# Optimization experiments

Hardware: AMD Instinct MI355X
Metric: run time of the kernel (lower is better)

The kernel has to match this reference:

```python
import jax, jax.numpy as jnp
import numpy as np

N, E, D, H, C = 100000, 1600000, 64, 8, 10
NEG_SLOPE = 0.2


def setup_inputs() -> dict:
    key = jax.random.key(0)
    ks = jax.random.split(key, 20)
    rn = lambda k, sh: jax.random.normal(k, sh, jnp.float32) * 0.1
    return dict(
        x=jax.random.normal(ks[0], (N, D), jnp.float32),
        edge_index=jax.random.randint(ks[1], (2, E), 0, N),
        gcnK_W=rn(ks[2], (D, D)), gcnK_b=rn(ks[3], (D,)),
        gcnV_W=rn(ks[4], (D, D)), gcnV_b=rn(ks[5], (D,)),
        super_Q=rn(ks[6], (C, D)),
        mha_in_w=rn(ks[7], (3 * D, D)), mha_in_b=rn(ks[8], (3 * D,)),
        mha_out_w=rn(ks[9], (D, D)), mha_out_b=rn(ks[10], (D,)),
        gat_W=rn(ks[11], (D, D)), gat_Wc=rn(ks[12], (D, D)),
        gat_a_src=rn(ks[13], (D,)), gat_a_dst=rn(ks[14], (D,)),
        gat_b=rn(ks[15], (D,)),
        t1_W=rn(ks[16], (D, 2 * D)), t1_b=rn(ks[17], (2 * D,)),
        t2_W=rn(ks[18], (2 * D, D)), t2_b=rn(ks[19], (D,)),
    )


def _gcn(x, W, b, src, dst, norm_e):
    # PyG GCNConv: symmetric-normalized aggregation over (A + I)
    h = x @ W  # [N, D]
    agg = jax.ops.segment_sum(h[src] * norm_e[:, None], dst, num_segments=N)
    return agg + b


def _mha(q, k, v, in_w, in_b, out_w, out_b):
    # torch.nn.MultiheadAttention (unbatched), eval mode (dropout off)
    L, n, hd = q.shape[0], k.shape[0], D // H
    Wq, Wk, Wv = jnp.split(in_w, 3, axis=0)
    bq, bk, bv = jnp.split(in_b, 3)
    scale = 1.0 / float(np.sqrt(hd))
    qh = ((q @ Wq.T + bq) * scale).reshape(L, H, hd).transpose(1, 0, 2)  # [H,L,hd]
    kh = (k @ Wk.T + bk).reshape(n, H, hd).transpose(1, 0, 2)            # [H,n,hd]
    vh = (v @ Wv.T + bv).reshape(n, H, hd).transpose(1, 0, 2)
    attn = jax.nn.softmax(jnp.einsum('hld,hnd->hln', qh, kh), axis=-1)
    o = jnp.einsum('hln,hnd->hld', attn, vh).transpose(1, 0, 2).reshape(L, D)
    return o @ out_w.T + out_b


def _context_gat(x, src, dst, context, W, Wc, a_src, a_dst, b):
    # context-conditioned GAT: per-edge logits use node terms + global context gate
    h = x @ W
    c = context @ Wc  # [D]
    s_src = h @ (a_src + c)  # context modulates source attention vector
    s_dst = h @ a_dst
    logits = jax.nn.leaky_relu(s_src[src] + s_dst[dst], NEG_SLOPE)  # [E]
    m = jax.ops.segment_max(logits, dst, num_segments=N)
    ex = jnp.exp(logits - m[dst])
    denom = jax.ops.segment_sum(ex, dst, num_segments=N)
    alpha = ex / (denom[dst] + 1e-16)
    out = jax.ops.segment_sum(alpha[:, None] * h[src], dst, num_segments=N)
    return out + b


def reference(x, edge_index, gcnK_W, gcnK_b, gcnV_W, gcnV_b, super_Q,
              mha_in_w, mha_in_b, mha_out_w, mha_out_b,
              gat_W, gat_Wc, gat_a_src, gat_a_dst, gat_b,
              t1_W, t1_b, t2_W, t2_b):
    src, dst = edge_index[0], edge_index[1]
    loop = jnp.arange(N)
    srcl = jnp.concatenate([src, loop])
    dstl = jnp.concatenate([dst, loop])
    deg = jax.ops.segment_sum(jnp.ones_like(srcl, jnp.float32), dstl, num_segments=N)
    dinv = jnp.where(deg > 0, 1.0 / jnp.sqrt(deg), 0.0)
    norm_e = dinv[srcl] * dinv[dstl]
    x_K = _gcn(x, gcnK_W, gcnK_b, srcl, dstl, norm_e)
    x_V = _gcn(x, gcnV_W, gcnV_b, srcl, dstl, norm_e)
    cluster = _mha(super_Q, x_K, x_V, mha_in_w, mha_in_b, mha_out_w, mha_out_b)  # [C, D]
    context = jnp.mean(cluster, axis=0)  # [D]
    g = _context_gat(x_V, src, dst, context, gat_W, gat_Wc, gat_a_src, gat_a_dst, gat_b)
    h1 = jax.nn.relu(g @ t1_W + t1_b)
    return jax.nn.relu(h1 @ t2_W + t2_b)
```

## Files before the change

### kernel.cpp

```cpp
#include <hip/hip_runtime.h>
#include <hip/hip_bf16.h>
#include <stdint.h>

#define NN 100000
#define EE 1600000
#define NBK 391
#define CHUNK 4096
#define NCB 98
#define NPROJ 1563
#define NS 32

#define FMA4(xi, vv, a, base)                      \
  a[(base)+0] = fmaf((xi), (vv).x, a[(base)+0]);   \
  a[(base)+1] = fmaf((xi), (vv).y, a[(base)+1]);   \
  a[(base)+2] = fmaf((xi), (vv).z, a[(base)+2]);   \
  a[(base)+3] = fmaf((xi), (vv).w, a[(base)+3]);

typedef __attribute__((ext_vector_type(8))) short bf16x8;
typedef __attribute__((ext_vector_type(4))) float f32x4;
typedef __attribute__((ext_vector_type(2))) float f32x2;
union FragU { uint4 u; bf16x8 h; };

__device__ inline unsigned pack_bf2(float a, float b) {
  __hip_bfloat162 t;
  t.x = __float2bfloat16(a);
  t.y = __float2bfloat16(b);
  return *reinterpret_cast<unsigned*>(&t);
}

__device__ inline f32x2 unpk2(unsigned u) {
  f32x2 r;
  r.x = __uint_as_float(u << 16);
  r.y = __uint_as_float(u & 0xffff0000u);
  return r;
}

__launch_bounds__(256)
__global__ void k_hist(const int* __restrict__ ei, int* __restrict__ histmat) {
  __shared__ int hist[NCB];
  int t = threadIdx.x;
  if (t < NCB) hist[t] = 0;
  __syncthreads();
  int base = blockIdx.x * CHUNK;
  int nb = EE - base; if (nb > CHUNK) nb = CHUNK;
  for (int k = t; k < nb; k += 256)
    atomicAdd(&hist[ei[EE + base + k] >> 10], 1);
  __syncthreads();
  if (t < NCB) histmat[blockIdx.x * NCB + t] = hist[t];
}

__launch_bounds__(256)
__global__ void k_sumcb(const int* __restrict__ histmat, int* __restrict__ cbsum) {
  __shared__ int red[4];
  int cb = blockIdx.x, t = threadIdx.x;
  int s = 0;
  for (int blk = t; blk < NBK; blk += 256) s += histmat[blk * NCB + cb];
#pragma unroll
  for (int off = 32; off > 0; off >>= 1) s += __shfl_down(s, off);
  if ((t & 63) == 0) red[t >> 6] = s;
  __syncthreads();
  if (t == 0) cbsum[cb] = red[0] + red[1] + red[2] + red[3];
}

__launch_bounds__(512)
__global__ void k_ppos(const int* __restrict__ histmat, const int* __restrict__ cbsum,
                       int* __restrict__ bstart, int* __restrict__ offsets,
                       int* __restrict__ ppos) {
  __shared__ int sm[512];
  __shared__ int sb[128];
  int cb = blockIdx.x, t = threadIdx.x;
  if (t < 128) sb[t] = (t < NCB) ? cbsum[t] : 0;
  __syncthreads();
  for (int off = 1; off < 128; off <<= 1) {
    int x = (t < 128 && t >= off) ? sb[t - off] : 0;
    __syncthreads();
    if (t < 128) sb[t] += x;
    __syncthreads();
  }
  int bs = (cb == 0) ? 0 : sb[cb - 1];
  if (t == 0) bstart[cb] = bs;
  if (cb == 0 && t == 0) { bstart[NCB] = EE; offsets[NN] = EE; }
  int v = (t < NBK) ? histmat[t * NCB + cb] : 0;
  sm[t] = v;
  __syncthreads();
  for (int off = 1; off < 512; off <<= 1) {
    int x = (t >= off) ? sm[t - off] : 0;
    __syncthreads();
    sm[t] += x;
    __syncthreads();
  }
  if (t < NBK) ppos[cb * NBK + t] = bs + sm[t] - v;
}

__launch_bounds__(256)
__global__ void k_fill_b(const int* __restrict__ ei, const int* __restrict__ ppos,
                         unsigned* __restrict__ brec) {
  __shared__ int hist[NCB], binstart[NCB], bincur[NCB], pbase[NCB];
  __shared__ unsigned lbuf[CHUNK];
  __shared__ unsigned char cbArr[CHUNK];
  int t = threadIdx.x;
  int base = blockIdx.x * CHUNK;
  int nb = EE - base; if (nb > CHUNK) nb = CHUNK;
  if (t < NCB) { hist[t] = 0; pbase[t] = ppos[t * NBK + blockIdx.x]; }
  __syncthreads();
  unsigned rec[16]; int rcb[16]; int cnt = 0;
  for (int k = t; k < nb; k += 256) {
    int s = ei[base + k], d = ei[EE + base + k];
    rec[cnt] = (unsigned)s | ((unsigned)(d & 1023) << 17);
    rcb[cnt] = d >> 10;
    atomicAdd(&hist[rcb[cnt]], 1);
    cnt++;
  }
  __syncthreads();
  if (t < NCB) binstart[t] = hist[t];
  __syncthreads();
  for (int off = 1; off < NCB; off <<= 1) {
    int v = (t < NCB && t >= off) ? binstart[t - off] : 0;
    __syncthreads();
    if (t < NCB) binstart[t] += v;
    __syncthreads();
  }
  if (t < NCB) { binstart[t] -= hist[t]; bincur[t] = 0; }
  __syncthreads();
  for (int i = 0; i < cnt; i++) {
    int c = rcb[i];
    int pos = atomicAdd(&bincur[c], 1);
    int p = binstart[c] + pos;
    lbuf[p] = rec[i];
    cbArr[p] = (unsigned char)c;
  }
  __syncthreads();
  for (int i = t; i < nb; i += 256) {
    int c = cbArr[i];
    brec[pbase[c] + (i - binstart[c])] = lbuf[i];
  }
}

__launch_bounds__(1024)
__global__ void k_fill_c(const unsigned* __restrict__ brec, const int* __restrict__ bstart,
                         int* __restrict__ csr, int* __restrict__ offsets,
                         float* __restrict__ dinv) {
  __shared__ int cnt[1024], sm[1024];
  int cbk = blockIdx.x, t = threadIdx.x;
  int nb0 = cbk << 10;
  int nn = NN - nb0; if (nn > 1024) nn = 1024;
  cnt[t] = 0;
  __syncthreads();
  int e0 = bstart[cbk], e1 = bstart[cbk + 1];
  for (int j = e0 + t; j < e1; j += 1024)
    atomicAdd(&cnt[brec[j] >> 17], 1);
  __syncthreads();
  int cv = cnt[t];
  sm[t] = cv;
  __syncthreads();
  for (int off = 1; off < 1024; off <<= 1) {
    int v = (t >= off) ? sm[t - off] : 0;
    __syncthreads();
    sm[t] += v;
    __syncthreads();
  }
  sm[t] -= cv;
  if (t < nn) {
    offsets[nb0 + t] = e0 + sm[t];
    dinv[nb0 + t] = rsqrtf((float)(cv + 1));
  }
  cnt[t] = 0;
  __syncthreads();
  for (int j = e0 + t; j < e1; j += 1024) {
    unsigned r = brec[j];
    int dl = r >> 17;
    int p = atomicAdd(&cnt[dl], 1);
    csr[e0 + sm[dl] + p] = r & 0x1FFFF;
  }
}

__global__ void k_prep(const float* __restrict__ x, const float* __restrict__ dinv,
                       unsigned* __restrict__ xbf2) {
  int i = blockIdx.x * 256 + threadIdx.x;
  if (i >= NN * 32) return;
  float dv = dinv[i >> 5];
  float2 v = ((const float2*)x)[i];
  xbf2[i] = pack_bf2(v.x * dv, v.y * dv);
}

__launch_bounds__(256)
__global__ void k_agg_x(const unsigned* __restrict__ xbf2, const int* __restrict__ offsets,
                        const int* __restrict__ csr, const float* __restrict__ dinv,
                        unsigned* __restrict__ axb) {
  int gid = blockIdx.x * 256 + threadIdx.x;
  int n = gid >> 6;
  if (n >= NN) return;
  int lane = gid & 63, q = lane & 7, grp = lane >> 3;
  int e0 = offsets[n], e1 = offsets[n + 1];
  float dv = dinv[n];
  f32x2 a2[4];
#pragma unroll
  for (int i = 0; i < 4; i++) a2[i] = (f32x2){0.f, 0.f};
  if (grp == 0) {
    uint4 u = ((const uint4*)(xbf2 + (size_t)n * 32))[q];
    unsigned uu[4] = {u.x, u.y, u.z, u.w};
#pragma unroll
    for (int p = 0; p < 4; p++) a2[p] += unpk2(uu[p]);
  }
  int b2 = e0;
  for (; b2 + 8 < e1; b2 += 16) {
    int j0 = b2 + grp, j1 = j0 + 8;
    int s0 = csr[j0];
    bool ok1 = j1 < e1;
    int s1 = ok1 ? csr[j1] : s0;
    uint4 u0 = ((const uint4*)(xbf2 + (size_t)s0 * 32))[q];
    uint4 u1 = ((const uint4*)(xbf2 + (size_t)s1 * 32))[q];
    unsigned w0[4] = {u0.x, u0.y, u0.z, u0.w};
    unsigned w1[4] = {u1.x, u1.y, u1.z, u1.w};
#pragma unroll
    for (int p = 0; p < 4; p++) a2[p] += unpk2(w0[p]);
    if (ok1) {
#pragma unroll
      for (int p = 0; p < 4; p++) a2[p] += unpk2(w1[p]);
    }
  }
  for (; b2 < e1; b2 += 8) {
    int j = b2 + grp;
    if (j < e1) {
      int s = csr[j];
      uint4 u = ((const uint4*)(xbf2 + (size_t)s * 32))[q];
      unsigned uu[4] = {u.x, u.y, u.z, u.w};
#pragma unroll
      for (int p = 0; p < 4; p++) a2[p] += unpk2(uu[p]);
    }
  }
#pragma unroll
  for (int i = 0; i < 4; i++) {
    a2[i].x += __shfl_xor(a2[i].x, 8);
    a2[i].x += __shfl_xor(a2[i].x, 16);
    a2[i].x += __shfl_xor(a2[i].x, 32);
    a2[i].y += __shfl_xor(a2[i].y, 8);
    a2[i].y += __shfl_xor(a2[i].y, 16);
    a2[i].y += __shfl_xor(a2[i].y, 32);
  }
  if (lane < 8) {
    uint4 u;
    u.x = pack_bf2(a2[0].x * dv, a2[0].y * dv);
    u.y = pack_bf2(a2[1].x * dv, a2[1].y * dv);
    u.z = pack_bf2(a2[2].x * dv, a2[2].y * dv);
    u.w = pack_bf2(a2[3].x * dv, a2[3].y * dv);
    ((uint4*)(axb + (size_t)n * 32))[q] = u;
  }
}

__launch_bounds__(256)
__global__ void k_fusew(const float* __restrict__ gcnK_W, const float* __restrict__ gcnK_b,
                        const float* __restrict__ gcnV_W, const float* __restrict__ gcnV_b,
                        const float* __restrict__ mha_in_w, const float* __restrict__ mha_in_b,
                        const float* __restrict__ gat_W, const float* __restrict__ sQ,
                        unsigned* __restrict__ Wt, float* __restrict__ bb) {
  __shared__ float sW1[64 * 65];
  __shared__ float sW2[64 * 65];
  __shared__ float sW3[64 * 65];
  __shared__ float sqq[640], qhs[640], Ms[5120], kb[64];
  int blk = blockIdx.x, t = threadIdx.x;
  const float scale = 0.35355339059327373f;
  if (blk < 16) {
    for (int i = t; i < 4096; i += 256) sW1[(i >> 6) * 65 + (i & 63)] = gcnV_W[i];
    if (blk < 8) {
      for (int i = t; i < 512; i += 256) sW2[i] = mha_in_w[(128 + blk * 8) * 64 + i];
    } else {
      for (int i = t; i < 4096; i += 256) sW2[(i >> 6) * 65 + (i & 63)] = gat_W[i];
    }
    __syncthreads();
    int idx = blk * 256 + t;
    int d = idx >> 5, kp = idx & 31;
    float v2[2];
#pragma unroll
    for (int u2 = 0; u2 < 2; u2++) {
      int k = kp * 2 + u2;
      float s = 0.f;
      if (d < 64) {
        int r = d & 7;
        for (int j = 0; j < 64; j++) s = fmaf(sW1[k * 65 + j], sW2[r * 64 + j], s);
      } else {
        int c = d - 64;
        for (int j = 0; j < 64; j++) s = fmaf(sW1[k * 65 + j], sW2[j * 65 + c], s);
      }
      v2[u2] = s;
    }
    Wt[idx] = pack_bf2(v2[0], v2[1]);
    if (t < 8) {
      if (blk < 8) {
        int d0 = blk * 8 + t;
        float s = mha_in_b[128 + d0];
        for (int j = 0; j < 64; j++) s = fmaf(gcnV_b[j], sW2[t * 64 + j], s);
        bb[d0] = s;
      } else {
        int c = (blk - 8) * 8 + t;
        float s = 0.f;
        for (int j = 0; j < 64; j++) s = fmaf(gcnV_b[j], sW2[j * 65 + c], s);
        bb[64 + c] = s;
      }
    }
  } else {
    for (int i = t; i < 4096; i += 256) {
      int r = i >> 6, c = i & 63;
      sW1[r * 65 + c] = gcnK_W[i];
      sW2[r * 65 + c] = mha_in_w[64 * 64 + i];
      sW3[r * 65 + c] = mha_in_w[i];
    }
    for (int i = t; i < 640; i += 256) sqq[i] = sQ[i];
    __syncthreads();
    for (int e = t; e < 640; e += 256) {
      int lv = e >> 6, c = e & 63;
      float acc = mha_in_b[c];
      for (int i = 0; i < 64; i++) acc = fmaf(sqq[lv * 64 + i], sW3[c * 65 + i], acc);
      qhs[e] = acc * scale;
    }
    if (t < 64) {
      float s = mha_in_b[64 + t];
      for (int j = 0; j < 64; j++) s = fmaf(gcnK_b[j], sW2[t * 65 + j], s);
      kb[t] = s;
    }
    __syncthreads();
    for (int e = t; e < 5120; e += 256) {
      int j = e / 80, hl = e % 80;
      int h = hl / 10, lv = hl % 10;
      float s = 0.f;
#pragma unroll
      for (int c = 0; c < 8; c++) {
        int cp = h * 8 + c;
        s = fmaf(sW2[cp * 65 + j], qhs[lv * 64 + cp], s);
      }
      Ms[j * 80 + hl] = s;
    }
    if (t < 80) {
      int h = t / 10, lv = t % 10;
      float s = 0.f;
#pragma unroll
      for (int c = 0; c < 8; c++) {
        int cp = h * 8 + c;
        s = fmaf(kb[cp], qhs[lv * 64 + cp], s);
      }
      bb[128 + t] = s;
    }
    __syncthreads();
    for (int e = t; e < 2560; e += 256) {
      int hl = e >> 5, kp = e & 31;
      float v2[2];
#pragma unroll
      for (int u2 = 0; u2 < 2; u2++) {
        int k = kp * 2 + u2;
        float s = 0.f;
        for (int j = 0; j < 64; j++) s = fmaf(sW1[k * 65 + j], Ms[j * 80 + hl], s);
        v2[u2] = s;
      }
      Wt[(128 + hl) * 32 + kp] = pack_bf2(v2[0], v2[1]);
    }
  }
}

__launch_bounds__(256)
__global__ void k_proj(const unsigned* __restrict__ axb, const unsigned* __restrict__ Wt,
                       const float* __restrict__ bb, const float* __restrict__ a_dst,
                       unsigned* __restrict__ hGb, float* __restrict__ s_dstv,
                       float* __restrict__ part) {
  __shared__ float red[4][720];
  int t = threadIdx.x;
  int wid = t >> 6, l = t & 63;
  int l15 = l & 15, lg = l >> 4;
  int base = blockIdx.x * 64;
  int rowbase = base + wid * 16;

  FragU a0, a1;
  {
    int r = rowbase + l15;
    if (r < NN) {
      const uint4* p = (const uint4*)(axb + (size_t)r * 32);
      a0.u = p[lg];
      a1.u = p[4 + lg];
    } else {
      a0.u = make_uint4(0u, 0u, 0u, 0u);
      a1.u = a0.u;
    }
  }
  f32x4 acc[13];
#pragma unroll
  for (int ct = 0; ct < 13; ct++) acc[ct] = (f32x4){0.f, 0.f, 0.f, 0.f};
#pragma unroll
  for (int ct = 0; ct < 13; ct++) {
    const uint4* wp = (const uint4*)(Wt + (size_t)(ct * 16 + l15) * 32);
    FragU b0, b1;
    b0.u = wp[lg];
    b1.u = wp[4 + lg];
    acc[ct] = __builtin_amdgcn_mfma_f32_16x16x32_bf16(a0.h, b0.h, acc[ct], 0, 0, 0);
    acc[ct] = __builtin_amdgcn_mfma_f32_16x16x32_bf16(a1.h, b1.h, acc[ct], 0, 0, 0);
  }

  float sdp[4] = {0.f, 0.f, 0.f, 0.f};
  __hip_bfloat16* hgp = (__hip_bfloat16*)hGb;
#pragma unroll
  for (int gt = 0; gt < 4; gt++) {
    int col = gt * 16 + l15;
    float bias = bb[64 + col];
    float ad = a_dst[col];
#pragma unroll
    for (int r = 0; r < 4; r++) {
      float hg = acc[4 + gt][r] + bias;
      sdp[r] = fmaf(hg, ad, sdp[r]);
      int row = rowbase + lg * 4 + r;
      if (row < NN) hgp[(size_t)row * 64 + col] = __float2bfloat16(hg);
    }
  }
#pragma unroll
  for (int r = 0; r < 4; r++) {
    float v = sdp[r];
    v += __shfl_xor(v, 1); v += __shfl_xor(v, 2);
    v += __shfl_xor(v, 4); v += __shfl_xor(v, 8);
    int row = rowbase + lg * 4 + r;
    if (l15 == 0 && row < NN) s_dstv[row] = v;
  }

  float wz[5][4];
#pragma unroll
  for (int zt = 0; zt < 5; zt++) {
    int zcol = zt * 16 + l15;
    float bias = bb[128 + zcol];
    float sp = 0.f;
#pragma unroll
    for (int r = 0; r < 4; r++) {
      int row = rowbase + lg * 4 + r;
      float z = acc[8 + zt][r] + bias;
      float w = (row < NN) ? __expf(z) : 0.f;
      wz[zt][r] = w;
      sp += w;
    }
    sp += __shfl_xor(sp, 16);
    sp += __shfl_xor(sp, 32);
    if (l < 16) {
      int h = zcol / 10, lv = zcol % 10;
      red[wid][h * 90 + lv] = sp;
    }
  }

  int sA = (l15 + 32 * lg) & 63;
  int sB2 = (sA + 16) & 63;
  bool loK = (lg < 2);
  FragU af[5];
#pragma unroll
  for (int zt = 0; zt < 5; zt++) {
    unsigned wlo = pack_bf2(wz[zt][0], wz[zt][1]);
    unsigned whi = pack_bf2(wz[zt][2], wz[zt][3]);
    unsigned f0 = __shfl(wlo, sA), f1 = __shfl(whi, sA);
    unsigned f2 = __shfl(wlo, sB2), f3 = __shfl(whi, sB2);
    af[zt].u.x = loK ? f0 : 0u;
    af[zt].u.y = loK ? f1 : 0u;
    af[zt].u.z = loK ? f2 : 0u;
    af[zt].u.w = loK ? f3 : 0u;
  }
#pragma unroll
  for (int vt = 0; vt < 4; vt++) {
    float bias = bb[vt * 16 + l15];
    unsigned vlo = pack_bf2(acc[vt][0] + bias, acc[vt][1] + bias);
    unsigned vhi = pack_bf2(acc[vt][2] + bias, acc[vt][3] + bias);
    FragU bf;
    {
      unsigned f0 = __shfl(vlo, sA), f1 = __shfl(vhi, sA);
      unsigned f2 = __shfl(vlo, sB2), f3 = __shfl(vhi, sB2);
      bf.u.x = loK ? f0 : 0u;
      bf.u.y = loK ? f1 : 0u;
      bf.u.z = loK ? f2 : 0u;
      bf.u.w = loK ? f3 : 0u;
    }
    f32x4 oacc[5];
#pragma unroll
    for (int zt = 0; zt < 5; zt++) {
      oacc[zt] = (f32x4){0.f, 0.f, 0.f, 0.f};
      oacc[zt] = __builtin_amdgcn_mfma_f32_16x16x32_bf16(af[zt].h, bf.h, oacc[zt], 0, 0, 0);
    }
#pragma unroll
    for (int zt = 0; zt < 5; zt++) {
#pragma unroll
      for (int r = 0; r < 4; r++) {
        int hl = zt * 16 + lg * 4 + r;
        int h = hl / 10, lv = hl - h * 10;
        if (vt * 2 + (l15 >> 3) == h)
          red[wid][h * 90 + 10 + lv * 8 + (l15 & 7)] = oacc[zt][r];
      }
    }
  }

  __syncthreads();
  for (int j = t; j < 720; j += 256) {
    float v = red[0][j] + red[1][j] + red[2][j] + red[3][j];
    part[(size_t)blockIdx.x * 720 + j] = v;
  }
}

__launch_bounds__(256)
__global__ void k_mred1(const float* __restrict__ part, float* __restrict__ part2) {
  int blk = blockIdx.x, t = threadIdx.x;
  int per = (NPROJ + NS - 1) / NS;
  int b0 = blk * per, b1 = b0 + per; if (b1 > NPROJ) b1 = NPROJ;
  float v0 = 0.f, v1 = 0.f, v2 = 0.f;
  for (int b = b0; b < b1; b++) {
    const float* row = part + (size_t)b * 720;
    v0 += row[t];
    if (t + 256 < 720) v1 += row[t + 256];
    if (t + 512 < 720) v2 += row[t + 512];
  }
  part2[(size_t)blk * 720 + t] = v0;
  if (t + 256 < 720) part2[(size_t)blk * 720 + t + 256] = v1;
  if (t + 512 < 720) part2[(size_t)blk * 720 + t + 512] = v2;
}

__global__ void k_context(const float* __restrict__ part2, const float* __restrict__ out_w,
                          const float* __restrict__ out_b, const float* __restrict__ a_src,
                          const float* __restrict__ gat_Wc, float* __restrict__ aeff) {
  __shared__ float po[640], cl[640], ctx[64], ac[720];
  int t = threadIdx.x;
  for (int j = t; j < 720; j += 640) {
    float v = 0.f;
#pragma unroll
    for (int s = 0; s < NS; s++) v += part2[(size_t)s * 720 + j];
    int cg = j / 90, r = j % 90;
    ac[(r < 10) ? (cg * 10 + r) : (80 + cg * 80 + (r - 10))] = v;
  }
  __syncthreads();
  {
    int h = t / 80, r = t % 80, l = r >> 3, j = r & 7;
    po[l * 64 + h * 8 + j] = ac[80 + t] / ac[h * 10 + l];
  }
  __syncthreads();
  {
    int l = t >> 6, d = t & 63;
    float v = out_b[d];
    for (int c = 0; c < 64; c++) v = fmaf(po[l * 64 + c], out_w[d * 64 + c], v);
    cl[t] = v;
  }
  __syncthreads();
  if (t < 64) {
    float m = 0.f;
#pragma unroll
    for (int l = 0; l < 10; l++) m += cl[l * 64 + t];
    ctx[t] = m * 0.1f;
  }
  __syncthreads();
  if (t < 64) {
    float v = a_src[t];
    for (int i = 0; i < 64; i++) v = fmaf(ctx[i], gat_Wc[i * 64 + t], v);
    aeff[t] = v;
  }
}

__launch_bounds__(256)
__global__ void k_ssrc(const unsigned* __restrict__ hGb, const float* __restrict__ aeff,
                       float* __restrict__ s_src) {
  int gid = blockIdx.x * 256 + threadIdx.x;
  int n = gid >> 6, lane = gid & 63;
  if (n >= NN) return;
  const __hip_bfloat16* hp = (const __hip_bfloat16*)hGb;
  float v = __bfloat162float(hp[(size_t)n * 64 + lane]) * aeff[lane];
#pragma unroll
  for (int off = 32; off > 0; off >>= 1) v += __shfl_xor(v, off);
  if (lane == 0) s_src[n] = v;
}

__launch_bounds__(256)
__global__ void k_gat(const int* __restrict__ offsets, const int* __restrict__ csr,
                      const float* __restrict__ s_src, const float* __restrict__ s_dstv,
                      const unsigned* __restrict__ hGb, const float* __restrict__ gat_b,
                      unsigned* __restrict__ gb) {
  int gid = blockIdx.x * 256 + threadIdx.x;
  int n = gid >> 6;
  if (n >= NN) return;
  int lane = gid & 63, q = lane & 7, grp = lane >> 3;
  int e0 = offsets[n], e1 = offsets[n + 1];
  float sd = s_dstv[n];
  float den = 0.f;
  f32x2 a2[4];
#pragma unroll
  for (int i = 0; i < 4; i++) a2[i] = (f32x2){0.f, 0.f};
  int b2 = e0;
  for (; b2 + 8 < e1; b2 += 16) {
    int j0 = b2 + grp, j1 = j0 + 8;
    int s0 = csr[j0];
    bool ok1 = j1 < e1;
    int s1 = ok1 ? csr[j1] : s0;
    float z0 = s_src[s0] + sd;
    float z1 = s_src[s1] + sd;
    uint4 u0 = ((const uint4*)(hGb + (size_t)s0 * 32))[q];
    uint4 u1 = ((const uint4*)(hGb + (size_t)s1 * 32))[q];
    unsigned w0[4] = {u0.x, u0.y, u0.z, u0.w};
    unsigned w1[4] = {u1.x, u1.y, u1.z, u1.w};
    z0 = z0 > 0.f ? z0 : 0.2f * z0;
    float ex0 = __expf(z0);
    den += ex0;
    f32x2 e0v = (f32x2){ex0, ex0};
#pragma unroll
    for (int p = 0; p < 4; p++) a2[p] = e0v * unpk2(w0[p]) + a2[p];
    if (ok1) {
      z1 = z1 > 0.f ? z1 : 0.2f * z1;
      float ex1 = __expf(z1);
      den += ex1;
      f32x2 e1v = (f32x2){ex1, ex1};
#pragma unroll
      for (int p = 0; p < 4; p++) a2[p] = e1v * unpk2(w1[p]) + a2[p];
    }
  }
  for (; b2 < e1; b2 += 8) {
    int j = b2 + grp;
    if (j < e1) {
      int s = csr[j];
      float z = s_src[s] + sd;
      z = z > 0.f ? z : 0.2f * z;
      float ex = __expf(z);
      den += ex;
      uint4 u = ((const uint4*)(hGb + (size_t)s * 32))[q];
      unsigned uu[4] = {u.x, u.y, u.z, u.w};
      f32x2 ev = (f32x2){ex, ex};
#pragma unroll
      for (int p = 0; p < 4; p++) a2[p] = ev * unpk2(uu[p]) + a2[p];
    }
  }
  den += __shfl_xor(den, 8);
  den += __shfl_xor(den, 16);
  den += __shfl_xor(den, 32);
#pragma unroll
  for (int i = 0; i < 4; i++) {
    a2[i].x += __shfl_xor(a2[i].x, 8);
    a2[i].x += __shfl_xor(a2[i].x, 16);
    a2[i].x += __shfl_xor(a2[i].x, 32);
    a2[i].y += __shfl_xor(a2[i].y, 8);
    a2[i].y += __shfl_xor(a2[i].y, 16);
    a2[i].y += __shfl_xor(a2[i].y, 32);
  }
  float inv = 1.f / (den + 1e-16f);
  if (lane < 8) {
    uint4 u;
    u.x = pack_bf2(a2[0].x * inv + gat_b[q * 8 + 0], a2[0].y * inv + gat_b[q * 8 + 1]);
    u.y = pack_bf2(a2[1].x * inv + gat_b[q * 8 + 2], a2[1].y * inv + gat_b[q * 8 + 3]);
    u.z = pack_bf2(a2[2].x * inv + gat_b[q * 8 + 4], a2[2].y * inv + gat_b[q * 8 + 5]);
    u.w = pack_bf2(a2[3].x * inv + gat_b[q * 8 + 6], a2[3].y * inv + gat_b[q * 8 + 7]);
    ((uint4*)(gb + (size_t)n * 32))[q] = u;
  }
}

__launch_bounds__(256)
__global__ void k_mlp1(const unsigned* __restrict__ gb, const float* __restrict__ W1,
                       const float* __restrict__ b1, unsigned* __restrict__ h1b) {
  __shared__ float sX[32 * 65];
  __shared__ float sW[64 * 128];
  __shared__ float sb[128];
  int t = threadIdx.x;
  int base = blockIdx.x * 32;
  for (int i = t; i < 8192; i += 256) sW[i] = W1[i];
  if (t < 128) sb[t] = b1[t];
  for (int idx = t; idx < 32 * 8; idx += 256) {
    int rl = idx >> 3, c8 = idx & 7;
    int row = base + rl;
    uint4 u = (row < NN) ? ((const uint4*)(gb + (size_t)row * 32))[c8]
                         : make_uint4(0u, 0u, 0u, 0u);
    unsigned uu[4] = {u.x, u.y, u.z, u.w};
    float* dst = sX + rl * 65 + c8 * 8;
#pragma unroll
    for (int p = 0; p < 4; p++) {
      __hip_bfloat162 v = *reinterpret_cast<__hip_bfloat162*>(&uu[p]);
      dst[2 * p] = __bfloat162float(v.x);
      dst[2 * p + 1] = __bfloat162float(v.y);
    }
  }
  __syncthreads();
  int cg = t & 15, rg = t >> 4;
  int r0 = rg * 2;
  float a0[8], a1[8];
#pragma unroll
  for (int i = 0; i < 8; i++) { a0[i] = 0.f; a1[i] = 0.f; }
  const float4* W4 = (const float4*)sW;
#pragma unroll 4
  for (int i = 0; i < 64; i++) {
    float x0 = sX[r0 * 65 + i];
    float x1 = sX[(r0 + 1) * 65 + i];
    float4 w0 = W4[i * 32 + cg * 2], w1 = W4[i * 32 + cg * 2 + 1];
    FMA4(x0, w0, a0, 0); FMA4(x0, w1, a0, 4);
    FMA4(x1, w0, a1, 0); FMA4(x1, w1, a1, 4);
  }
#pragma unroll
  for (int r = 0; r < 2; r++) {
    int row = base + r0 + r;
    if (row >= NN) continue;
    float* a = r ? a1 : a0;
    float h[8];
#pragma unroll
    for (int c = 0; c < 8; c++) h[c] = fmaxf(a[c] + sb[cg * 8 + c], 0.f);
    uint4 u;
    u.x = pack_bf2(h[0], h[1]);
    u.y = pack_bf2(h[2], h[3]);
    u.z = pack_bf2(h[4], h[5]);
    u.w = pack_bf2(h[6], h[7]);
    ((uint4*)(h1b + (size_t)row * 64))[cg] = u;
  }
}

__launch_bounds__(256)
__global__ void k_mlp2(const unsigned* __restrict__ h1b, const float* __restrict__ W2,
                       const float* __restrict__ b2, float* __restrict__ out) {
  __shared__ unsigned sH[64 * 65];
  __shared__ float sW[128 * 64];
  __shared__ float sb[64];
  int t = threadIdx.x;
  int base = blockIdx.x * 64;
  for (int i = t; i < 8192; i += 256) sW[i] = W2[i];
  if (t < 64) sb[t] = b2[t];
  for (int idx = t; idx < 64 * 16; idx += 256) {
    int rl = idx >> 4, c4 = idx & 15;
    int row = base + rl;
    uint4 v = (row < NN) ? ((const uint4*)h1b)[(size_t)row * 16 + c4]
                         : make_uint4(0u, 0u, 0u, 0u);
    sH[rl * 65 + 4 * c4 + 0] = v.x;
    sH[rl * 65 + 4 * c4 + 1] = v.y;
    sH[rl * 65 + 4 * c4 + 2] = v.z;
    sH[rl * 65 + 4 * c4 + 3] = v.w;
  }
  __syncthreads();
  int cg = t & 7, rg = t >> 3;
  int r0 = rg * 2;
  float a0[8], a1[8];
#pragma unroll
  for (int i = 0; i < 8; i++) { a0[i] = 0.f; a1[i] = 0.f; }
  const float4* W4 = (const float4*)sW;
#pragma unroll 2
  for (int kp = 0; kp < 64; kp++) {
    unsigned u0 = sH[r0 * 65 + kp];
    unsigned u1 = sH[(r0 + 1) * 65 + kp];
    float x0a = __uint_as_float(u0 << 16), x0b = __uint_as_float(u0 & 0xffff0000u);
    float x1a = __uint_as_float(u1 << 16), x1b = __uint_as_float(u1 & 0xffff0000u);
    int k0 = 2 * kp, k1 = 2 * kp + 1;
    float4 wa0 = W4[k0 * 16 + cg * 2], wa1 = W4[k0 * 16 + cg * 2 + 1];
    float4 wb0 = W4[k1 * 16 + cg * 2], wb1 = W4[k1 * 16 + cg * 2 + 1];
    FMA4(x0a, wa0, a0, 0); FMA4(x0a, wa1, a0, 4);
    FMA4(x0b, wb0, a0, 0); FMA4(x0b, wb1, a0, 4);
    FMA4(x1a, wa0, a1, 0); FMA4(x1a, wa1, a1, 4);
    FMA4(x1b, wb0, a1, 0); FMA4(x1b, wb1, a1, 4);
  }
#pragma unroll
  for (int r = 0; r < 2; r++) {
    int row = base + r0 + r;
    if (row >= NN) continue;
    float* a = r ? a1 : a0;
    float4* op = (float4*)(out + (size_t)row * 64 + cg * 8);
    op[0] = make_float4(fmaxf(a[0] + sb[cg * 8 + 0], 0.f), fmaxf(a[1] + sb[cg * 8 + 1], 0.f),
                        fmaxf(a[2] + sb[cg * 8 + 2], 0.f), fmaxf(a[3] + sb[cg * 8 + 3], 0.f));
    op[1] = make_float4(fmaxf(a[4] + sb[cg * 8 + 4], 0.f), fmaxf(a[5] + sb[cg * 8 + 5], 0.f),
                        fmaxf(a[6] + sb[cg * 8 + 6], 0.f), fmaxf(a[7] + sb[cg * 8 + 7], 0.f));
  }
}

extern "C" void kernel_launch(void* const* d_in, const int* in_sizes, int n_in,
                              void* d_out, int out_size, void* d_ws, size_t ws_size,
                              hipStream_t stream) {
  (void)in_sizes; (void)n_in; (void)out_size; (void)ws_size;
  const float* x        = (const float*)d_in[0];
  const int*   ei       = (const int*)d_in[1];
  const float* gcnK_W   = (const float*)d_in[2];
  const float* gcnK_b   = (const float*)d_in[3];
  const float* gcnV_W   = (const float*)d_in[4];
  const float* gcnV_b   = (const float*)d_in[5];
  const float* super_Q  = (const float*)d_in[6];
  const float* mha_in_w = (const float*)d_in[7];
  const float* mha_in_b = (const float*)d_in[8];
  const float* mha_out_w= (const float*)d_in[9];
  const float* mha_out_b= (const float*)d_in[10];
  const float* gat_W    = (const float*)d_in[11];
  const float* gat_Wc   = (const float*)d_in[12];
  const float* gat_a_src= (const float*)d_in[13];
  const float* gat_a_dst= (const float*)d_in[14];
  const float* gat_b    = (const float*)d_in[15];
  const float* t1_W     = (const float*)d_in[16];
  const float* t1_b     = (const float*)d_in[17];
  const float* t2_W     = (const float*)d_in[18];
  const float* t2_b     = (const float*)d_in[19];

  char* ws = (char*)d_ws;
  size_t cur = 0;
  auto alloc = [&](size_t bytes) -> char* {
    char* p = ws + cur;
    cur = (cur + bytes + 255) & ~(size_t)255;
    return p;
  };
  int*      histmat = (int*)alloc((size_t)NBK * NCB * 4);
  int*      cbsum   = (int*)alloc((size_t)NCB * 4);
  int*      ppos    = (int*)alloc((size_t)NCB * NBK * 4);
  int*      bstart  = (int*)alloc((size_t)(NCB + 1) * 4);
  int*      offsets = (int*)alloc((size_t)(NN + 1) * 4);
  float*    dinv    = (float*)alloc((size_t)NN * 4);
  int*      csr     = (int*)alloc((size_t)EE * 4);
  unsigned* brec    = (unsigned*)alloc((size_t)EE * 4);
  unsigned* Wt      = (unsigned*)alloc((size_t)208 * 32 * 4);
  float*    bb      = (float*)alloc(208 * 4);
  float*    aeff    = (float*)alloc(64 * 4);
  float*    part    = (float*)alloc((size_t)NPROJ * 720 * 4);
  float*    part2   = (float*)alloc((size_t)NS * 720 * 4);
  float*    s_src   = (float*)alloc((size_t)NN * 4);
  float*    s_dstv  = (float*)alloc((size_t)NN * 4);
  unsigned* xbf     = (unsigned*)alloc((size_t)NN * 128);
  unsigned* axb     = (unsigned*)alloc((size_t)NN * 128);
  unsigned* hGb     = (unsigned*)alloc((size_t)NN * 128);
  unsigned* gb      = (unsigned*)alloc((size_t)NN * 128);
  unsigned* h1b     = (unsigned*)alloc((size_t)NN * 64 * 4);
  float*    g       = (float*)d_out;

  k_hist<<<NBK, 256, 0, stream>>>(ei, histmat);
  k_sumcb<<<NCB, 256, 0, stream>>>(histmat, cbsum);
  k_ppos<<<NCB, 512, 0, stream>>>(histmat, cbsum, bstart, offsets, ppos);
  k_fill_b<<<NBK, 256, 0, stream>>>(ei, ppos, brec);
  k_fill_c<<<NCB, 1024, 0, stream>>>(brec, bstart, csr, offsets, dinv);
  k_prep<<<(NN * 32 + 255) / 256, 256, 0, stream>>>(x, dinv, xbf);
  k_agg_x<<<NN / 4, 256, 0, stream>>>(xbf, offsets, csr, dinv, axb);
  k_fusew<<<17, 256, 0, stream>>>(gcnK_W, gcnK_b, gcnV_W, gcnV_b, mha_in_w, mha_in_b,
                                  gat_W, super_Q, Wt, bb);
  k_proj<<<NPROJ, 256, 0, stream>>>(axb, Wt, bb, gat_a_dst, hGb, s_dstv, part);
  k_mred1<<<NS, 256, 0, stream>>>(part, part2);
  k_context<<<1, 640, 0, stream>>>(part2, mha_out_w, mha_out_b, gat_a_src, gat_Wc, aeff);
  k_ssrc<<<NN / 4, 256, 0, stream>>>(hGb, aeff, s_src);
  k_gat<<<NN / 4, 256, 0, stream>>>(offsets, csr, s_src, s_dstv, hGb, gat_b, gb);
  k_mlp1<<<(NN + 31) / 32, 256, 0, stream>>>(gb, t1_W, t1_b, h1b);
  k_mlp2<<<(NN + 63) / 64, 256, 0, stream>>>(h1b, t2_W, t2_b, g);
}
```

Baseline: 423.8 us.

## Gather GAT features in fp8 and use lane-per-feature aggregation loops

k_proj now also writes an fp8 copy of the GAT projection, and k_gat gathers that copy instead of the bf16 one, halving the bytes moved per edge. Both k_agg_x and k_gat are restructured so each of the 64 lanes owns one feature column and walks the edge list serially, unrolled by four, which removes the cross-lane shuffle reductions. The cost is fp8 quantization error on the GAT aggregation, scalar 1–2 byte loads instead of 16-byte vector loads, and an extra write pass for the fp8 buffer.

```diff
diff --git a/kernel.cpp b/kernel.cpp
--- a/kernel.cpp
+++ b/kernel.cpp
@@ -28,11 +28,8 @@
   return *reinterpret_cast<unsigned*>(&t);
 }
 
-__device__ inline f32x2 unpk2(unsigned u) {
-  f32x2 r;
-  r.x = __uint_as_float(u << 16);
-  r.y = __uint_as_float(u & 0xffff0000u);
-  return r;
+__device__ inline float bf2f(unsigned short u) {
+  return __uint_as_float(((unsigned)u) << 16);
 }
 
 __launch_bounds__(256)
@@ -190,62 +187,25 @@
   int gid = blockIdx.x * 256 + threadIdx.x;
   int n = gid >> 6;
   if (n >= NN) return;
-  int lane = gid & 63, q = lane & 7, grp = lane >> 3;
+  int lane = gid & 63;
+  const unsigned short* xb = (const unsigned short*)xbf2;
   int e0 = offsets[n], e1 = offsets[n + 1];
   float dv = dinv[n];
-  f32x2 a2[4];
-#pragma unroll
-  for (int i = 0; i < 4; i++) a2[i] = (f32x2){0.f, 0.f};
-  if (grp == 0) {
-    uint4 u = ((const uint4*)(xbf2 + (size_t)n * 32))[q];
-    unsigned uu[4] = {u.x, u.y, u.z, u.w};
-#pragma unroll
-    for (int p = 0; p < 4; p++) a2[p] += unpk2(uu[p]);
-  }
-  int b2 = e0;
-  for (; b2 + 8 < e1; b2 += 16) {
-    int j0 = b2 + grp, j1 = j0 + 8;
-    int s0 = csr[j0];
-    bool ok1 = j1 < e1;
-    int s1 = ok1 ? csr[j1] : s0;
-    uint4 u0 = ((const uint4*)(xbf2 + (size_t)s0 * 32))[q];
-    uint4 u1 = ((const uint4*)(xbf2 + (size_t)s1 * 32))[q];
-    unsigned w0[4] = {u0.x, u0.y, u0.z, u0.w};
-    unsigned w1[4] = {u1.x, u1.y, u1.z, u1.w};
-#pragma unroll
-    for (int p = 0; p < 4; p++) a2[p] += unpk2(w0[p]);
-    if (ok1) {
-#pragma unroll
-      for (int p = 0; p < 4; p++) a2[p] += unpk2(w1[p]);
-    }
-  }
-  for (; b2 < e1; b2 += 8) {
-    int j = b2 + grp;
-    if (j < e1) {
-      int s = csr[j];
-      uint4 u = ((const uint4*)(xbf2 + (size_t)s * 32))[q];
-      unsigned uu[4] = {u.x, u.y, u.z, u.w};
-#pragma unroll
-      for (int p = 0; p < 4; p++) a2[p] += unpk2(uu[p]);
-    }
-  }
-#pragma unroll
-  for (int i = 0; i < 4; i++) {
-    a2[i].x += __shfl_xor(a2[i].x, 8);
-    a2[i].x += __shfl_xor(a2[i].x, 16);
-    a2[i].x += __shfl_xor(a2[i].x, 32);
-    a2[i].y += __shfl_xor(a2[i].y, 8);
-    a2[i].y += __shfl_xor(a2[i].y, 16);
-    a2[i].y += __shfl_xor(a2[i].y, 32);
-  }
-  if (lane < 8) {
-    uint4 u;
-    u.x = pack_bf2(a2[0].x * dv, a2[0].y * dv);
-    u.y = pack_bf2(a2[1].x * dv, a2[1].y * dv);
-    u.z = pack_bf2(a2[2].x * dv, a2[2].y * dv);
-    u.w = pack_bf2(a2[3].x * dv, a2[3].y * dv);
-    ((uint4*)(axb + (size_t)n * 32))[q] = u;
-  }
+  float acc = bf2f(xb[(size_t)n * 64 + lane]);
+  int j = e0;
+  for (; j + 3 < e1; j += 4) {
+    int s0 = csr[j], s1 = csr[j + 1], s2 = csr[j + 2], s3 = csr[j + 3];
+    float v0 = bf2f(xb[(size_t)s0 * 64 + lane]);
+    float v1 = bf2f(xb[(size_t)s1 * 64 + lane]);
+    float v2 = bf2f(xb[(size_t)s2 * 64 + lane]);
+    float v3 = bf2f(xb[(size_t)s3 * 64 + lane]);
+    acc += v0 + v1 + v2 + v3;
+  }
+  for (; j < e1; j++) {
+    int s = csr[j];
+    acc += bf2f(xb[(size_t)s * 64 + lane]);
+  }
+  ((__hip_bfloat16*)axb)[(size_t)n * 64 + lane] = __float2bfloat16(acc * dv);
 }
 
 __launch_bounds__(256)
@@ -359,8 +319,8 @@
 __launch_bounds__(256)
 __global__ void k_proj(const unsigned* __restrict__ axb, const unsigned* __restrict__ Wt,
                        const float* __restrict__ bb, const float* __restrict__ a_dst,
-                       unsigned* __restrict__ hGb, float* __restrict__ s_dstv,
-                       float* __restrict__ part) {
+                       unsigned* __restrict__ hGb, unsigned char* __restrict__ hG8,
+                       float* __restrict__ s_dstv, float* __restrict__ part) {
   __shared__ float red[4][720];
   int t = threadIdx.x;
   int wid = t >> 6, l = t & 63;
@@ -405,7 +365,11 @@
       float hg = acc[4 + gt][r] + bias;
       sdp[r] = fmaf(hg, ad, sdp[r]);
       int row = rowbase + lg * 4 + r;
-      if (row < NN) hgp[(size_t)row * 64 + col] = __float2bfloat16(hg);
+      if (row < NN) {
+        hgp[(size_t)row * 64 + col] = __float2bfloat16(hg);
+        unsigned wq = __builtin_amdgcn_cvt_pk_fp8_f32(hg, hg, 0u, false);
+        hG8[(size_t)row * 64 + col] = (unsigned char)(wq & 0xffu);
+      }
     }
   }
 #pragma unroll
@@ -565,81 +529,47 @@
 __launch_bounds__(256)
 __global__ void k_gat(const int* __restrict__ offsets, const int* __restrict__ csr,
                       const float* __restrict__ s_src, const float* __restrict__ s_dstv,
-                      const unsigned* __restrict__ hGb, const float* __restrict__ gat_b,
+                      const unsigned char* __restrict__ hG8, const float* __restrict__ gat_b,
                       unsigned* __restrict__ gb) {
   int gid = blockIdx.x * 256 + threadIdx.x;
   int n = gid >> 6;
   if (n >= NN) return;
-  int lane = gid & 63, q = lane & 7, grp = lane >> 3;
+  int lane = gid & 63;
   int e0 = offsets[n], e1 = offsets[n + 1];
   float sd = s_dstv[n];
   float den = 0.f;
-  f32x2 a2[4];
-#pragma unroll
-  for (int i = 0; i < 4; i++) a2[i] = (f32x2){0.f, 0.f};
-  int b2 = e0;
-  for (; b2 + 8 < e1; b2 += 16) {
-    int j0 = b2 + grp, j1 = j0 + 8;
-    int s0 = csr[j0];
-    bool ok1 = j1 < e1;
-    int s1 = ok1 ? csr[j1] : s0;
-    float z0 = s_src[s0] + sd;
-    float z1 = s_src[s1] + sd;
-    uint4 u0 = ((const uint4*)(hGb + (size_t)s0 * 32))[q];
-    uint4 u1 = ((const uint4*)(hGb + (size_t)s1 * 32))[q];
-    unsigned w0[4] = {u0.x, u0.y, u0.z, u0.w};
-    unsigned w1[4] = {u1.x, u1.y, u1.z, u1.w};
+  float acc = 0.f;
+  int j = e0;
+  for (; j + 3 < e1; j += 4) {
+    int s0 = csr[j], s1 = csr[j + 1], s2 = csr[j + 2], s3 = csr[j + 3];
+    unsigned b0 = hG8[(size_t)s0 * 64 + lane];
+    unsigned b1 = hG8[(size_t)s1 * 64 + lane];
+    unsigned b2 = hG8[(size_t)s2 * 64 + lane];
+    unsigned b3 = hG8[(size_t)s3 * 64 + lane];
+    float z0 = s_src[s0] + sd, z1 = s_src[s1] + sd;
+    float z2 = s_src[s2] + sd, z3 = s_src[s3] + sd;
     z0 = z0 > 0.f ? z0 : 0.2f * z0;
-    float ex0 = __expf(z0);
-    den += ex0;
-    f32x2 e0v = (f32x2){ex0, ex0};
-#pragma unroll
-    for (int p = 0; p < 4; p++) a2[p] = e0v * unpk2(w0[p]) + a2[p];
-    if (ok1) {
-      z1 = z1 > 0.f ? z1 : 0.2f * z1;
-      float ex1 = __expf(z1);
-      den += ex1;
-      f32x2 e1v = (f32x2){ex1, ex1};
-#pragma unroll
-      for (int p = 0; p < 4; p++) a2[p] = e1v * unpk2(w1[p]) + a2[p];
-    }
-  }
-  for (; b2 < e1; b2 += 8) {
-    int j = b2 + grp;
-    if (j < e1) {
-      int s = csr[j];
-      float z = s_src[s] + sd;
-      z = z > 0.f ? z : 0.2f * z;
-      float ex = __expf(z);
-      den += ex;
-      uint4 u = ((const uint4*)(hGb + (size_t)s * 32))[q];
-      unsigned uu[4] = {u.x, u.y, u.z, u.w};
-      f32x2 ev = (f32x2){ex, ex};
-#pragma unroll
-      for (int p = 0; p < 4; p++) a2[p] = ev * unpk2(uu[p]) + a2[p];
-    }
-  }
-  den += __shfl_xor(den, 8);
-  den += __shfl_xor(den, 16);
-  den += __shfl_xor(den, 32);
-#pragma unroll
-  for (int i = 0; i < 4; i++) {
-    a2[i].x += __shfl_xor(a2[i].x, 8);
-    a2[i].x += __shfl_xor(a2[i].x, 16);
-    a2[i].x += __shfl_xor(a2[i].x, 32);
-    a2[i].y += __shfl_xor(a2[i].y, 8);
-    a2[i].y += __shfl_xor(a2[i].y, 16);
-    a2[i].y += __shfl_xor(a2[i].y, 32);
+    z1 = z1 > 0.f ? z1 : 0.2f * z1;
+    z2 = z2 > 0.f ? z2 : 0.2f * z2;
+    z3 = z3 > 0.f ? z3 : 0.2f * z3;
+    float ex0 = __expf(z0), ex1 = __expf(z1), ex2 = __expf(z2), ex3 = __expf(z3);
+    den += (ex0 + ex1) + (ex2 + ex3);
+    acc = fmaf(ex0, __builtin_amdgcn_cvt_f32_fp8(b0, 0), acc);
+    acc = fmaf(ex1, __builtin_amdgcn_cvt_f32_fp8(b1, 0), acc);
+    acc = fmaf(ex2, __builtin_amdgcn_cvt_f32_fp8(b2, 0), acc);
+    acc = fmaf(ex3, __builtin_amdgcn_cvt_f32_fp8(b3, 0), acc);
+  }
+  for (; j < e1; j++) {
+    int s = csr[j];
+    unsigned b = hG8[(size_t)s * 64 + lane];
+    float z = s_src[s] + sd;
+    z = z > 0.f ? z : 0.2f * z;
+    float ex = __expf(z);
+    den += ex;
+    acc = fmaf(ex, __builtin_amdgcn_cvt_f32_fp8(b, 0), acc);
   }
   float inv = 1.f / (den + 1e-16f);
-  if (lane < 8) {
-    uint4 u;
-    u.x = pack_bf2(a2[0].x * inv + gat_b[q * 8 + 0], a2[0].y * inv + gat_b[q * 8 + 1]);
-    u.y = pack_bf2(a2[1].x * inv + gat_b[q * 8 + 2], a2[1].y * inv + gat_b[q * 8 + 3]);
-    u.z = pack_bf2(a2[2].x * inv + gat_b[q * 8 + 4], a2[2].y * inv + gat_b[q * 8 + 5]);
-    u.w = pack_bf2(a2[3].x * inv + gat_b[q * 8 + 6], a2[3].y * inv + gat_b[q * 8 + 7]);
-    ((uint4*)(gb + (size_t)n * 32))[q] = u;
-  }
+  ((__hip_bfloat16*)gb)[(size_t)n * 64 + lane] = __float2bfloat16(acc * inv + gat_b[lane]);
 }
 
 __launch_bounds__(256)
@@ -802,6 +732,7 @@
   unsigned* xbf     = (unsigned*)alloc((size_t)NN * 128);
   unsigned* axb     = (unsigned*)alloc((size_t)NN * 128);
   unsigned* hGb     = (unsigned*)alloc((size_t)NN * 128);
+  unsigned char* hG8 = (unsigned char*)alloc((size_t)NN * 64);
   unsigned* gb      = (unsigned*)alloc((size_t)NN * 128);
   unsigned* h1b     = (unsigned*)alloc((size_t)NN * 64 * 4);
   float*    g       = (float*)d_out;
@@ -815,11 +746,11 @@
   k_agg_x<<<NN / 4, 256, 0, stream>>>(xbf, offsets, csr, dinv, axb);
   k_fusew<<<17, 256, 0, stream>>>(gcnK_W, gcnK_b, gcnV_W, gcnV_b, mha_in_w, mha_in_b,
                                   gat_W, super_Q, Wt, bb);
-  k_proj<<<NPROJ, 256, 0, stream>>>(axb, Wt, bb, gat_a_dst, hGb, s_dstv, part);
+  k_proj<<<NPROJ, 256, 0, stream>>>(axb, Wt, bb, gat_a_dst, hGb, hG8, s_dstv, part);
   k_mred1<<<NS, 256, 0, stream>>>(part, part2);
   k_context<<<1, 640, 0, stream>>>(part2, mha_out_w, mha_out_b, gat_a_src, gat_Wc, aeff);
   k_ssrc<<<NN / 4, 256, 0, stream>>>(hGb, aeff, s_src);
-  k_gat<<<NN / 4, 256, 0, stream>>>(offsets, csr, s_src, s_dstv, hGb, gat_b, gb);
+  k_gat<<<NN / 4, 256, 0, stream>>>(offsets, csr, s_src, s_dstv, hG8, gat_b, gb);
   k_mlp1<<<(NN + 31) / 32, 256, 0, stream>>>(gb, t1_W, t1_b, h1b);
   k_mlp2<<<(NN + 63) / 64, 256, 0, stream>>>(h1b, t2_W, t2_b, g);
 }
```

Measured after the change: 470.6 us. 11.0% more time.
